# Kernel optimization log

Hardware: AMD Instinct MI355X
Metric: run time of the kernel (lower is better)

## Reference

```python
import jax, jax.numpy as jnp
import numpy as np

NEG_INF = -1e30  # stands in for torch's -inf diagonal mask; exp() underflows to 0 identically


def conv1x1(x, w, b):
    # x: [B,C,H,W], w: [O,C], b: [O]
    return jnp.einsum('oc,bchw->bohw', w, x) + b[None, :, None, None]


def s_module(x, qw, qb, kw, kb, vw, vb, gamma):
    # CCNet criss-cross attention with -inf diagonal masking on the H branch.
    B, C, H, W = x.shape
    q = conv1x1(x, qw, qb)  # [B,C8,H,W]
    k = conv1x1(x, kw, kb)  # [B,C8,H,W]
    v = conv1x1(x, vw, vb)  # [B,C,H,W]
    # energy_H[b,h,w,g] = <q[b,:,h,w], k[b,:,g,w]>  (attend along column)
    e_h = jnp.einsum('bchw,bcgw->bhwg', q, k)
    diag_mask = jnp.where(jnp.eye(H, dtype=bool), NEG_INF, 0.0).astype(x.dtype)
    e_h = e_h + diag_mask[None, :, None, :]  # mask h == g
    # energy_W[b,h,w,v] = <q[b,:,h,w], k[b,:,h,v]>  (attend along row)
    e_w = jnp.einsum('bchw,bchv->bhwv', q, k)
    att = jax.nn.softmax(jnp.concatenate([e_h, e_w], axis=-1), axis=-1)  # [B,H,W,H+W]
    a_h, a_w = att[..., :H], att[..., H:]
    out_h = jnp.einsum('bcgw,bhwg->bchw', v, a_h)
    out_w = jnp.einsum('bchv,bhwv->bchw', v, a_w)
    return gamma * (out_h + out_w) + x


def cam_module(x, fb, gamma):
    # channel attention: energy [B,C,C], max-sub trick, softmax, bmm back
    B, C, H, W = x.shape
    f = fb.reshape(B, C, H * W)
    energy = jnp.einsum('bcn,bdn->bcd', f, f)
    energy_new = jnp.max(energy, axis=-1, keepdims=True) - energy
    att = jax.nn.softmax(energy_new, axis=-1)
    out = jnp.einsum('bcd,bdn->bcn', att, f).reshape(B, C, H, W)
    return x + gamma * out


def _forward(x, fb, w_conv, b_conv, bn_g, bn_b,
             xq_w, xq_b, xk_w, xk_b, xv_w, xv_b, x_gamma,
             fq_w, fq_b, fk_w, fk_b, fv_w, fv_b, f_gamma,
             pam_gamma, pam_gamma2, cam_gamma):
    # MaxPool2d(kernel=2, stride=2)
    fbd = jax.lax.reduce_window(fb, -jnp.inf, jax.lax.max,
                                (1, 1, 2, 2), (1, 1, 2, 2), 'VALID')
    # convblock: 1x1 conv + BatchNorm (training-mode batch stats) + ReLU
    y = conv1x1(fbd, w_conv, b_conv)
    mu = jnp.mean(y, axis=(0, 2, 3), keepdims=True)
    var = jnp.var(y, axis=(0, 2, 3), keepdims=True)
    y = (y - mu) * jax.lax.rsqrt(var + 1e-5)
    y = y * bn_g[None, :, None, None] + bn_b[None, :, None, None]
    y = jax.nn.relu(y)
    # FeedbackSpatialAttention (PAM)
    x_att = pam_gamma * s_module(x, xq_w, xq_b, xk_w, xk_b, xv_w, xv_b, x_gamma)
    fb_att = s_module(y, fq_w, fq_b, fk_w, fk_b, fv_w, fv_b, f_gamma)
    pam_out = x + x_att + pam_gamma2 * fb_att
    # CAM on (x, processed fb)
    cam_out = cam_module(x, y, cam_gamma)
    return pam_out + cam_out


def setup_inputs() -> dict:
    key = jax.random.key(0)
    ks = jax.random.split(key, 24)
    B, C, H, W = 4, 64, 128, 128
    C8 = C // 8
    d = {
        'x': jax.random.normal(ks[0], (B, C, H, W), jnp.float32),
        'fb': jax.random.normal(ks[1], (B, C, 2 * H, 2 * W), jnp.float32),
        'w_conv': jax.random.normal(ks[2], (C, C), jnp.float32) * 0.05,
        'b_conv': jax.random.normal(ks[3], (C,), jnp.float32) * 0.02,
        'bn_g': jax.random.uniform(ks[4], (C,), jnp.float32, 0.5, 1.5),
        'bn_b': jax.random.normal(ks[5], (C,), jnp.float32) * 0.02,
        'xq_w': jax.random.normal(ks[6], (C8, C), jnp.float32) * 0.05,
        'xq_b': jax.random.normal(ks[7], (C8,), jnp.float32) * 0.02,
        'xk_w': jax.random.normal(ks[8], (C8, C), jnp.float32) * 0.05,
        'xk_b': jax.random.normal(ks[9], (C8,), jnp.float32) * 0.02,
        'xv_w': jax.random.normal(ks[10], (C, C), jnp.float32) * 0.05,
        'xv_b': jax.random.normal(ks[11], (C,), jnp.float32) * 0.02,
        'x_gamma': jax.random.normal(ks[12], (1,), jnp.float32) * 0.1,
        'fq_w': jax.random.normal(ks[13], (C8, C), jnp.float32) * 0.05,
        'fq_b': jax.random.normal(ks[14], (C8,), jnp.float32) * 0.02,
        'fk_w': jax.random.normal(ks[15], (C8, C), jnp.float32) * 0.05,
        'fk_b': jax.random.normal(ks[16], (C8,), jnp.float32) * 0.02,
        'fv_w': jax.random.normal(ks[17], (C, C), jnp.float32) * 0.05,
        'fv_b': jax.random.normal(ks[18], (C,), jnp.float32) * 0.02,
        'f_gamma': jax.random.normal(ks[19], (1,), jnp.float32) * 0.1,
        'pam_gamma': jax.random.normal(ks[20], (1,), jnp.float32) * 0.1,
        'pam_gamma2': jax.random.normal(ks[21], (1,), jnp.float32) * 0.1,
        'cam_gamma': jax.random.normal(ks[22], (1,), jnp.float32) * 0.1,
    }
    return d


def reference(x, fb, w_conv, b_conv, bn_g, bn_b,
              xq_w, xq_b, xk_w, xk_b, xv_w, xv_b, x_gamma,
              fq_w, fq_b, fk_w, fk_b, fv_w, fv_b, f_gamma,
              pam_gamma, pam_gamma2, cam_gamma):
    return _forward(x, fb, w_conv, b_conv, bn_g, bn_b,
                    xq_w, xq_b, xk_w, xk_b, xv_w, xv_b, x_gamma,
                    fq_w, fq_b, fk_w, fk_b, fv_w, fv_b, f_gamma,
                    pam_gamma, pam_gamma2, cam_gamma)
```

## Files before the change

### kernel.cpp

```cpp
#include <hip/hip_runtime.h>
#include <hip/hip_bf16.h>

#define NP 16384
#define NB 4

typedef __hip_bfloat16 bf16;
typedef unsigned short u16;
typedef unsigned short us8 __attribute__((ext_vector_type(8)));
typedef short ss8 __attribute__((ext_vector_type(8)));
typedef float f32x4 __attribute__((ext_vector_type(4)));
__device__ __forceinline__ float bf2f(const bf16 v) { return __bfloat162float(v); }
__device__ __forceinline__ bf16 f2bf(float v) { return __float2bfloat16(v); }
__device__ __forceinline__ float bfu(u16 h) {
  return __uint_as_float(((unsigned)h) << 16);
}
__device__ __forceinline__ u16 fbu(float v) {
  bf16 b = f2bf(v);
  return *(u16*)&b;
}


__global__ __launch_bounds__(256) void k_pool_conv(
    const float* __restrict__ fb, const float* __restrict__ wconv,
    const float* __restrict__ bconv, bf16* __restrict__ Y) {
  __shared__ float wS[64 * 65], bS[64], Xs[4096];
  int tid = threadIdx.x;
  int b = blockIdx.x >> 8, tile = blockIdx.x & 255;
  int n0 = tile * 64;
  for (int i = tid; i < 4096; i += 256) wS[(i >> 6) * 65 + (i & 63)] = wconv[i];
  if (tid < 64) bS[tid] = bconv[tid];
  for (int i = tid; i < 4096; i += 256) {
    int c = i >> 6, px = i & 63;
    int n = n0 + px, h = n >> 7, w = n & 127;
    size_t fbase = ((size_t)((b * 64 + c) * 256 + 2 * h)) * 256 + 2 * w;
    float2 v01 = *(const float2*)(fb + fbase);
    float2 v23 = *(const float2*)(fb + fbase + 256);
    Xs[i] = fmaxf(fmaxf(v01.x, v01.y), fmaxf(v23.x, v23.y));
  }
  __syncthreads();
  int ty = tid >> 4, tx = tid & 15;
  float acc[4][4];
#pragma unroll
  for (int i = 0; i < 4; ++i) {
    float bv = bS[ty + 16 * i];
#pragma unroll
    for (int j = 0; j < 4; ++j) acc[i][j] = bv;
  }
  for (int c = 0; c < 64; ++c) {
    float xv[4], wv[4];
#pragma unroll
    for (int j = 0; j < 4; ++j) xv[j] = Xs[c * 64 + tx * 4 + j];
#pragma unroll
    for (int i = 0; i < 4; ++i) wv[i] = wS[(ty + 16 * i) * 65 + c];
#pragma unroll
    for (int i = 0; i < 4; ++i)
#pragma unroll
      for (int j = 0; j < 4; ++j) acc[i][j] = fmaf(wv[i], xv[j], acc[i][j]);
  }
#pragma unroll
  for (int i = 0; i < 4; ++i) {
    int ch = ty + 16 * i;
    bf16* yb = Y + (size_t)(b * 64 + ch) * NP + n0 + tx * 4;
#pragma unroll
    for (int j = 0; j < 4; ++j) yb[j] = f2bf(acc[i][j]);
  }
}

__global__ __launch_bounds__(256) void k_stats_p1(const bf16* __restrict__ Y,
                                                  float* __restrict__ PS) {
  int blk = blockIdx.x, tid = threadIdx.x;
  int o = blk >> 3, slab = blk & 7;
  int b = slab >> 1, half = slab & 1;
  const us8* vp =
      (const us8*)(Y + ((size_t)(b * 64 + o)) * NP + half * 8192);
  float s = 0.f, ss = 0.f;
#pragma unroll
  for (int it = 0; it < 4; ++it) {
    us8 v = vp[tid + 256 * it];
#pragma unroll
    for (int e = 0; e < 8; ++e) {
      float f = bfu(v[e]);
      s += f;
      ss = fmaf(f, f, ss);
    }
  }
  for (int off = 32; off > 0; off >>= 1) {
    s += __shfl_down(s, off, 64);
    ss += __shfl_down(ss, off, 64);
  }
  __shared__ float sh[8];
  int wv = tid >> 6, ln = tid & 63;
  if (ln == 0) { sh[wv] = s; sh[4 + wv] = ss; }
  __syncthreads();
  if (tid == 0) {
    PS[blk] = sh[0] + sh[1] + sh[2] + sh[3];
    PS[512 + blk] = sh[4] + sh[5] + sh[6] + sh[7];
  }
}

__global__ __launch_bounds__(64) void k_stats_p2(
    const float* __restrict__ PS, const float* __restrict__ bng,
    const float* __restrict__ bnb, float* __restrict__ SCALE,
    float* __restrict__ SHIFT, const float* xg, const float* fg,
    const float* pg, const float* pg2, const float* cg,
    float* __restrict__ HDR) {
  int o = threadIdx.x;
  float s = 0.f, ss = 0.f;
#pragma unroll
  for (int k = 0; k < 8; ++k) {
    s += PS[o * 8 + k];
    ss += PS[512 + o * 8 + k];
  }
  const float inv = 1.0f / (NB * NP);
  float mu = s * inv;
  float var = ss * inv - mu * mu;
  float r = rsqrtf(var + 1e-5f);
  float sc = r * bng[o];
  SCALE[o] = sc;
  SHIFT[o] = bnb[o] - mu * sc;
  if (o == 0) {
    float vpg = pg[0];
    HDR[1] = vpg * xg[0];
    HDR[2] = pg2[0] * fg[0];
    HDR[3] = 2.0f + vpg;
    HDR[4] = pg2[0];
    HDR[5] = cg[0];
  }
}

__global__ __launch_bounds__(256) void k_conv80x2(
    const float* __restrict__ xin, const bf16* __restrict__ Yin,
    const float* __restrict__ SCALE, const float* __restrict__ SHIFT,
    const float* __restrict__ qw0, const float* __restrict__ qb0,
    const float* __restrict__ kw0, const float* __restrict__ kb0,
    const float* __restrict__ vw0, const float* __restrict__ vb0,
    const float* __restrict__ qw1, const float* __restrict__ qb1,
    const float* __restrict__ kw1, const float* __restrict__ kb1,
    const float* __restrict__ vw1, const float* __restrict__ vb1,
    bf16* __restrict__ QK, bf16* __restrict__ V) {
  __shared__ float wS[80 * 65], bS[80];
  __shared__ u16 Xs[4096];
  int tid = threadIdx.x;
  int m = blockIdx.x >> 10;
  int rest = blockIdx.x & 1023;
  int b = rest >> 8, tile = rest & 255;
  int n0 = tile * 64;
  const float* qw = m ? qw1 : qw0;
  const float* qb = m ? qb1 : qb0;
  const float* kw = m ? kw1 : kw0;
  const float* kb = m ? kb1 : kb0;
  const float* vw = m ? vw1 : vw0;
  const float* vb = m ? vb1 : vb0;
  for (int i = tid; i < 512; i += 256) {
    wS[(i >> 6) * 65 + (i & 63)] = qw[i];
    wS[(8 + (i >> 6)) * 65 + (i & 63)] = kw[i];
  }
  for (int i = tid; i < 4096; i += 256)
    wS[(16 + (i >> 6)) * 65 + (i & 63)] = vw[i];
  if (tid < 8) { bS[tid] = qb[tid]; bS[8 + tid] = kb[tid]; }
  if (tid < 64) bS[16 + tid] = vb[tid];
  for (int i = tid; i < 4096; i += 256) {
    int c = i >> 6, px = i & 63;
    size_t idx = (size_t)(b * 64 + c) * NP + n0 + px;
    float v;
    if (m) {
      v = bf2f(Yin[idx]);
      v = fmaf(v, SCALE[c], SHIFT[c]);
      v = fmaxf(v, 0.f);
    } else {
      v = xin[idx];
    }
    Xs[i] = fbu(v);
  }
  __syncthreads();
  int ty = tid >> 4, tx = tid & 15;
  float acc[5][4];
#pragma unroll
  for (int i = 0; i < 5; ++i) {
    float bv = bS[ty + 16 * i];
#pragma unroll
    for (int j = 0; j < 4; ++j) acc[i][j] = bv;
  }
  for (int c = 0; c < 64; ++c) {
    float xv[4], wv[5];
#pragma unroll
    for (int j = 0; j < 4; ++j) xv[j] = bfu(Xs[c * 64 + tx * 4 + j]);
#pragma unroll
    for (int i = 0; i < 5; ++i) wv[i] = wS[(ty + 16 * i) * 65 + c];
#pragma unroll
    for (int i = 0; i < 5; ++i)
#pragma unroll
      for (int j = 0; j < 4; ++j) acc[i][j] = fmaf(wv[i], xv[j], acc[i][j]);
  }
#pragma unroll
  for (int i = 0; i < 5; ++i) {
    int ch = ty + 16 * i;
    bf16* dst;
    size_t base;
    if (ch < 8) {
      dst = QK; base = (size_t)(((m * 2 + 0) * 4 + b) * 8 + ch) * NP;
    } else if (ch < 16) {
      dst = QK; base = (size_t)(((m * 2 + 1) * 4 + b) * 8 + (ch - 8)) * NP;
    } else {
      dst = V; base = (size_t)((m * 4 + b) * 64 + (ch - 16)) * NP;
    }
#pragma unroll
    for (int j = 0; j < 4; ++j) dst[base + n0 + tx * 4 + j] = f2bf(acc[i][j]);
  }
}

__global__ __launch_bounds__(256) void k_transpose2(
    const u16* __restrict__ inA, u16* __restrict__ outA,
    const u16* __restrict__ inB, u16* __restrict__ outB, int nA) {
  int tileId = blockIdx.x & 15;
  int plane = blockIdx.x >> 4;
  const u16* ip;
  u16* op;
  if (plane < nA) {
    ip = inA + (size_t)plane * NP;
    op = outA + (size_t)plane * NP;
  } else {
    ip = inB + (size_t)(plane - nA) * NP;
    op = outB + (size_t)(plane - nA) * NP;
  }
  int th = tileId >> 2, tw = tileId & 3;
  __shared__ u16 t[32][33];
  int lx = threadIdx.x & 31, ly = threadIdx.x >> 5;
  for (int i = 0; i < 32; i += 8)
    t[ly + i][lx] = ip[(size_t)(th * 32 + ly + i) * 128 + tw * 32 + lx];
  __syncthreads();
  for (int i = 0; i < 32; i += 8)
    op[(size_t)(tw * 32 + ly + i) * 128 + th * 32 + lx] = t[lx][ly + i];
}

__global__ __launch_bounds__(256, 4) void k_av(
    const bf16* __restrict__ QK, const bf16* __restrict__ QKT,
    const bf16* __restrict__ V, const bf16* __restrict__ VT,
    float* __restrict__ MWp, float* __restrict__ LWp,
    float* __restrict__ MHp, float* __restrict__ LHp,
    float* __restrict__ OW, bf16* __restrict__ OHT) {
  int blk = blockIdx.x;
  int m = blk & 1, mode = (blk >> 1) & 1;
  int bid = blk >> 2;
  int b = bid >> 7, h = bid & 127;
  const bf16* qkbase = mode ? QKT : QK;
  const bf16* Qp = qkbase + (size_t)(((m * 2 + 0) * 4 + b) * 8) * NP;
  const bf16* Kp = qkbase + (size_t)(((m * 2 + 1) * 4 + b) * 8) * NP;
  const bf16* Vp = (mode ? VT : V) + (size_t)((m * 4 + b) * 64) * NP;
  __shared__ __align__(16) u16 qT[128 * 8];
  __shared__ __align__(16) u16 kT[128 * 8];
  __shared__ __align__(16) u16 Vs[64 * 136];
  int tid = threadIdx.x;
  {
    int c = (tid >> 4) & 7, vj = tid & 15;
    const bf16* src = (tid < 128) ? Qp : Kp;
    u16* dst = (tid < 128) ? qT : kT;
    const us8* sp = (const us8*)(src + (size_t)c * NP + (size_t)h * 128);
    us8 sv = sp[vj];
#pragma unroll
    for (int e = 0; e < 8; ++e) {
      int j = vj * 8 + e;
      int p = ((j & 7) << 4) | (j >> 3);
      dst[p * 8 + c] = sv[e];
    }
  }
  for (int i2 = tid; i2 < 1024; i2 += 256) {
    int c = i2 >> 4, vj = i2 & 15;
    const us8* vp = (const us8*)(Vp + (size_t)c * NP + (size_t)h * 128);
    us8 vv = vp[vj];
    *(us8*)&Vs[c * 136 + vj * 8] = vv;
  }
  __syncthreads();
  int lane = tid & 63, wv = tid >> 6;
  int il = lane & 15, gq = lane >> 4;
  size_t sb = (size_t)(m * 4 + b) * NP;
  float* owBase = OW + (size_t)((m * 4 + b) * 64) * NP + (size_t)h * 128;
  bf16* ohBase = OHT + (size_t)((m * 4 + b) * 64) * NP + (size_t)h * 128;
#pragma unroll
  for (int sub = 0; sub < 2; ++sub) {
    int ib = wv * 32 + sub * 16;
    int i = ib + il;
    int pi = ((i & 7) << 4) | (i >> 3);
    us8 qv = *(const us8*)&qT[pi * 8];
    float qr[8];
#pragma unroll
    for (int c = 0; c < 8; ++c) qr[c] = bfu(qv[c]);
    float scr[4][8];
    float mrow = -3.0e38f;
#pragma unroll
    for (int ks = 0; ks < 4; ++ks) {
#pragma unroll
      for (int e = 0; e < 8; ++e) {
        int j = ks * 32 + gq * 8 + e;
        int pj = ((j & 7) << 4) | (j >> 3);
        us8 kv = *(const us8*)&kT[pj * 8];
        float s = 0.f;
#pragma unroll
        for (int c = 0; c < 8; ++c) s = fmaf(qr[c], bfu(kv[c]), s);
        if (mode && j == i) s = -1.0e30f;
        scr[ks][e] = s;
        mrow = fmaxf(mrow, s);
      }
    }
    mrow = fmaxf(mrow, __shfl_xor(mrow, 16, 64));
    mrow = fmaxf(mrow, __shfl_xor(mrow, 32, 64));
    float l = 0.f;
    ss8 afr[4];
#pragma unroll
    for (int ks = 0; ks < 4; ++ks) {
      ss8 af;
#pragma unroll
      for (int e = 0; e < 8; ++e) {
        float ev = __expf(scr[ks][e] - mrow);
        l += ev;
        af[e] = (short)fbu(ev);
      }
      afr[ks] = af;
    }
    l += __shfl_xor(l, 16, 64);
    l += __shfl_xor(l, 32, 64);
    if (gq == 0) {
      if (mode == 0) {
        MWp[sb + (size_t)h * 128 + i] = mrow;
        LWp[sb + (size_t)h * 128 + i] = l;
      } else {
        MHp[sb + (size_t)i * 128 + h] = mrow;
        LHp[sb + (size_t)i * 128 + h] = l;
      }
    }
#pragma unroll
    for (int ct = 0; ct < 4; ++ct) {
      f32x4 acc = {0.f, 0.f, 0.f, 0.f};
#pragma unroll
      for (int ks = 0; ks < 4; ++ks) {
        ss8 bv = *(const ss8*)&Vs[(ct * 16 + il) * 136 + ks * 32 + gq * 8];
        acc = __builtin_amdgcn_mfma_f32_16x16x32_bf16(afr[ks], bv, acc, 0, 0, 0);
      }
      int cch = ct * 16 + il;
      int i0 = ib + gq * 4;
      if (mode == 0) {
#pragma unroll
        for (int r = 0; r < 4; ++r)
          owBase[(size_t)cch * NP + (size_t)(i0 + r)] = acc[r];
      } else {
#pragma unroll
        for (int r = 0; r < 4; ++r)
          ohBase[(size_t)cch * NP + (size_t)(i0 + r)] = f2bf(acc[r]);
      }
    }
  }
}

__global__ __launch_bounds__(256) void k_merge2(
    const bf16* __restrict__ OHT, const float* __restrict__ OW,
    const float* __restrict__ MWp, const float* __restrict__ LWp,
    const float* __restrict__ MHp, const float* __restrict__ LHp,
    const float* __restrict__ HDR, float* __restrict__ ACC) {
  int tileId = blockIdx.x & 15;
  int plane = blockIdx.x >> 4;
  int b = plane >> 6;
  int th = tileId >> 2, tw = tileId & 3;
  __shared__ float t0[32][33], t1[32][33];
  int lx = threadIdx.x & 31, ly = threadIdx.x >> 5;
  const bf16* ip0 = OHT + (size_t)plane * NP;
  const bf16* ip1 = OHT + (size_t)(256 + plane) * NP;
  for (int i = 0; i < 32; i += 8) {
    size_t idx = (size_t)(th * 32 + ly + i) * 128 + tw * 32 + lx;
    t0[ly + i][lx] = bf2f(ip0[idx]);
    t1[ly + i][lx] = bf2f(ip1[idx]);
  }
  __syncthreads();
  float sc0 = HDR[1], sc1 = HDR[2];
  float* op = ACC + (size_t)plane * NP;
  const float* ow0 = OW + (size_t)plane * NP;
  const float* ow1 = OW + (size_t)(256 + plane) * NP;
  size_t s0 = (size_t)b * NP, s1 = (size_t)(4 + b) * NP;
  for (int i = 0; i < 32; i += 8) {
    int hh = tw * 32 + ly + i, ww = th * 32 + lx;
    size_t idx = (size_t)hh * 128 + ww;
    float mw0 = MWp[s0 + idx], mh0 = MHp[s0 + idx];
    float M0 = fmaxf(mw0, mh0);
    float ea0 = __expf(mw0 - M0), eb0 = __expf(mh0 - M0);
    float inv0 = 1.0f / (LWp[s0 + idx] * ea0 + LHp[s0 + idx] * eb0);
    float v0 = (ea0 * ow0[idx] + eb0 * t0[lx][ly + i]) * inv0;
    float mw1 = MWp[s1 + idx], mh1 = MHp[s1 + idx];
    float M1 = fmaxf(mw1, mh1);
    float ea1 = __expf(mw1 - M1), eb1 = __expf(mh1 - M1);
    float inv1 = 1.0f / (LWp[s1 + idx] * ea1 + LHp[s1 + idx] * eb1);
    float v1 = (ea1 * ow1[idx] + eb1 * t1[lx][ly + i]) * inv1;
    op[idx] = sc0 * v0 + sc1 * v1;
  }
}

__global__ __launch_bounds__(256) void k_gram(const bf16* __restrict__ Y,
                                              const float* __restrict__ SCALE,
                                              const float* __restrict__ SHIFT,
                                              float* __restrict__ GP) {
  int b = blockIdx.x >> 7, ch = (blockIdx.x >> 2) & 31, t = blockIdx.x & 3;
  int tid = threadIdx.x;
  __shared__ float fs[64 * 129];
  int cg = tid >> 4, dg = tid & 15;
  float acc[4][4];
#pragma unroll
  for (int i = 0; i < 4; ++i)
#pragma unroll
    for (int jx = 0; jx < 4; ++jx) acc[i][jx] = 0.f;
  const bf16* yb = Y + (size_t)b * 64 * NP + ch * 512;
  for (int idx = tid; idx < 8192; idx += 256) {
    int c = idx >> 7, j = idx & 127;
    float v = fmaf(bf2f(yb[(size_t)c * NP + t * 128 + j]), SCALE[c], SHIFT[c]);
    fs[c * 129 + j] = fmaxf(v, 0.f);
  }
  __syncthreads();
  for (int j = 0; j < 128; ++j) {
    float a[4], d[4];
#pragma unroll
    for (int i = 0; i < 4; ++i) a[i] = fs[(cg * 4 + i) * 129 + j];
#pragma unroll
    for (int i = 0; i < 4; ++i) d[i] = fs[(dg * 4 + i) * 129 + j];
#pragma unroll
    for (int i = 0; i < 4; ++i)
#pragma unroll
      for (int jx = 0; jx < 4; ++jx) acc[i][jx] = fmaf(a[i], d[jx], acc[i][jx]);
  }
  float* gp = GP + ((size_t)(b * 128) + ch * 4 + t) * 4096;
#pragma unroll
  for (int i = 0; i < 4; ++i)
#pragma unroll
    for (int jx = 0; jx < 4; ++jx)
      gp[(cg * 4 + i) * 64 + dg * 4 + jx] = acc[i][jx];
}

__global__ __launch_bounds__(256) void k_gram_reduce(const float* __restrict__ GP,
                                                     float* __restrict__ CATT) {
  int b = blockIdx.x >> 4, rg = blockIdx.x & 15;
  int tid = threadIdx.x;
  __shared__ float Es[256];
  int e = rg * 256 + tid;
  float s = 0.f;
  for (int k = 0; k < 128; ++k) s += GP[((size_t)b * 128 + k) * 4096 + e];
  Es[tid] = s;
  __syncthreads();
  int wv = tid >> 6, ln = tid & 63;
  float v = Es[wv * 64 + ln];
  float mn = v;
  for (int off = 32; off; off >>= 1) mn = fminf(mn, __shfl_xor(mn, off, 64));
  float ev = __expf(mn - v);
  float ssum = ev;
  for (int off = 32; off; off >>= 1) ssum += __shfl_xor(ssum, off, 64);
  CATT[((size_t)b * 64 + rg * 4 + wv) * 64 + ln] = ev / ssum;
}

__global__ __launch_bounds__(256) void k_final(
    const float* __restrict__ x, const bf16* __restrict__ Y,
    const float* __restrict__ SCALE, const float* __restrict__ SHIFT,
    const float* __restrict__ CATT, const float* __restrict__ HDR,
    float* __restrict__ OUT) {
  __shared__ float attS[64 * 65], Ys[64 * 65];
  int tid = threadIdx.x;
  int b = blockIdx.x >> 8, tile = blockIdx.x & 255;
  int n0 = tile * 64;
  for (int i = tid; i < 4096; i += 256)
    attS[(i >> 6) * 65 + (i & 63)] = CATT[(size_t)b * 4096 + i];
  for (int i = tid; i < 4096; i += 256) {
    int d = i >> 6, px = i & 63;
    float v = fmaf(bf2f(Y[(size_t)(b * 64 + d) * NP + n0 + px]), SCALE[d], SHIFT[d]);
    Ys[d * 65 + px] = fmaxf(v, 0.f);
  }
  __syncthreads();
  int cg = tid >> 4, pgx = tid & 15;
  int c0 = cg * 4, p0 = pgx * 4;
  float acc[4][4];
#pragma unroll
  for (int i = 0; i < 4; ++i)
#pragma unroll
    for (int j = 0; j < 4; ++j) acc[i][j] = 0.f;
  for (int d = 0; d < 64; ++d) {
    float a[4], yv[4];
#pragma unroll
    for (int i = 0; i < 4; ++i) a[i] = attS[(c0 + i) * 65 + d];
#pragma unroll
    for (int j = 0; j < 4; ++j) yv[j] = Ys[d * 65 + p0 + j];
#pragma unroll
    for (int i = 0; i < 4; ++i)
#pragma unroll
      for (int j = 0; j < 4; ++j) acc[i][j] = fmaf(a[i], yv[j], acc[i][j]);
  }
  float c2pg = HDR[3], fpg2 = HDR[4], fcg = HDR[5];
#pragma unroll
  for (int i = 0; i < 4; ++i) {
    size_t base = (size_t)(b * 64 + c0 + i) * NP + n0 + p0;
#pragma unroll
    for (int j = 0; j < 4; ++j) {
      float yv = Ys[(c0 + i) * 65 + p0 + j];
      OUT[base + j] =
          c2pg * x[base + j] + fpg2 * yv + OUT[base + j] + fcg * acc[i][j];
    }
  }
}

extern "C" void kernel_launch(void* const* d_in, const int* in_sizes, int n_in,
                              void* d_out, int out_size, void* d_ws, size_t ws_size,
                              hipStream_t stream) {
  const float* x = (const float*)d_in[0];
  const float* fbp = (const float*)d_in[1];

  char* base = (char*)d_ws;
  float* HDR = (float*)base;
  float* SCALE = HDR + 16;
  float* SHIFT = SCALE + 64;
  char* p = base + 4096;
  bf16* Y = (bf16*)p;    p += 8388608;
  bf16* QK = (bf16*)p;   p += 4194304;
  bf16* QKT = (bf16*)p;  p += 4194304;
  bf16* V = (bf16*)p;    p += 16777216;
  bf16* VT = (bf16*)p;   p += 16777216;
  float* MWp = (float*)p; p += 524288;
  float* LWp = (float*)p; p += 524288;
  float* MHp = (float*)p; p += 524288;
  float* LHp = (float*)p; p += 524288;
  bf16* OHT = (bf16*)p;  p += 16777216;
  float* OW = (float*)p; p += 33554432;
  float* GP = (float*)p; p += 8388608;
  float* CATT = (float*)p; p += 1048576;
  float* ACC = (float*)d_out;
  float* PS = (float*)QK;

  k_pool_conv<<<1024, 256, 0, stream>>>(fbp, (const float*)d_in[2],
                                        (const float*)d_in[3], Y);
  k_stats_p1<<<512, 256, 0, stream>>>(Y, PS);
  k_stats_p2<<<1, 64, 0, stream>>>(PS, (const float*)d_in[4],
                                   (const float*)d_in[5], SCALE, SHIFT,
                                   (const float*)d_in[12], (const float*)d_in[19],
                                   (const float*)d_in[20], (const float*)d_in[21],
                                   (const float*)d_in[22], HDR);

  k_conv80x2<<<2048, 256, 0, stream>>>(
      x, Y, SCALE, SHIFT,
      (const float*)d_in[6], (const float*)d_in[7], (const float*)d_in[8],
      (const float*)d_in[9], (const float*)d_in[10], (const float*)d_in[11],
      (const float*)d_in[13], (const float*)d_in[14], (const float*)d_in[15],
      (const float*)d_in[16], (const float*)d_in[17], (const float*)d_in[18],
      QK, V);
  k_transpose2<<<10240, 256, 0, stream>>>((const u16*)QK, (u16*)QKT,
                                          (const u16*)V, (u16*)VT, 128);
  k_av<<<2048, 256, 0, stream>>>(QK, QKT, V, VT, MWp, LWp, MHp, LHp, OW, OHT);
  k_merge2<<<4096, 256, 0, stream>>>(OHT, OW, MWp, LWp, MHp, LHp, HDR, ACC);

  k_gram<<<512, 256, 0, stream>>>(Y, SCALE, SHIFT, GP);
  k_gram_reduce<<<64, 256, 0, stream>>>(GP, CATT);
  k_final<<<1024, 256, 0, stream>>>(x, Y, SCALE, SHIFT, CATT, HDR,
                                    (float*)d_out);
}
```

Before: 301.3 us.

## Rewrite fused QKV 1x1 conv with bf16 MFMA and hi/lo split weights

Replaces the scalar-FMA 80-output 1x1 conv kernel with one using MFMA 16x16x32 bf16 instructions. Weights are split into hi and lo bf16 parts to keep near-fp32 weight precision. Activations are staged in XOR-swizzled LDS with vectorized global loads, and each block covers 128 pixels so the grid is halved. Stores are vectorized 4-wide. The aim is to cut the VALU-bound conv cost, in exchange for extra LDS and swizzle complexity.

```diff
diff --git a/kernel.cpp b/kernel.cpp
--- a/kernel.cpp
+++ b/kernel.cpp
@@ -7,6 +7,7 @@
 typedef __hip_bfloat16 bf16;
 typedef unsigned short u16;
 typedef unsigned short us8 __attribute__((ext_vector_type(8)));
+typedef unsigned short us4 __attribute__((ext_vector_type(4)));
 typedef short ss8 __attribute__((ext_vector_type(8)));
 typedef float f32x4 __attribute__((ext_vector_type(4)));
 __device__ __forceinline__ float bf2f(const bf16 v) { return __bfloat162float(v); }
@@ -128,7 +129,7 @@
   }
 }
 
-__global__ __launch_bounds__(256) void k_conv80x2(
+__global__ __launch_bounds__(256, 4) void k_conv_mfma(
     const float* __restrict__ xin, const bf16* __restrict__ Yin,
     const float* __restrict__ SCALE, const float* __restrict__ SHIFT,
     const float* __restrict__ qw0, const float* __restrict__ qb0,
@@ -138,74 +139,102 @@
     const float* __restrict__ kw1, const float* __restrict__ kb1,
     const float* __restrict__ vw1, const float* __restrict__ vb1,
     bf16* __restrict__ QK, bf16* __restrict__ V) {
-  __shared__ float wS[80 * 65], bS[80];
-  __shared__ u16 Xs[4096];
+  __shared__ __align__(16) u16 Xs[128 * 64];
+  __shared__ __align__(16) u16 wHi[80 * 64], wLo[80 * 64];
+  __shared__ float bS[80];
   int tid = threadIdx.x;
-  int m = blockIdx.x >> 10;
-  int rest = blockIdx.x & 1023;
-  int b = rest >> 8, tile = rest & 255;
-  int n0 = tile * 64;
+  int m = blockIdx.x >> 9;
+  int b = (blockIdx.x >> 7) & 3;
+  int tile = blockIdx.x & 127;
+  int n0 = tile * 128;
   const float* qw = m ? qw1 : qw0;
   const float* qb = m ? qb1 : qb0;
   const float* kw = m ? kw1 : kw0;
   const float* kb = m ? kb1 : kb0;
   const float* vw = m ? vw1 : vw0;
   const float* vb = m ? vb1 : vb0;
-  for (int i = tid; i < 512; i += 256) {
-    wS[(i >> 6) * 65 + (i & 63)] = qw[i];
-    wS[(8 + (i >> 6)) * 65 + (i & 63)] = kw[i];
-  }
-  for (int i = tid; i < 4096; i += 256)
-    wS[(16 + (i >> 6)) * 65 + (i & 63)] = vw[i];
-  if (tid < 8) { bS[tid] = qb[tid]; bS[8 + tid] = kb[tid]; }
-  if (tid < 64) bS[16 + tid] = vb[tid];
-  for (int i = tid; i < 4096; i += 256) {
-    int c = i >> 6, px = i & 63;
-    size_t idx = (size_t)(b * 64 + c) * NP + n0 + px;
-    float v;
-    if (m) {
-      v = bf2f(Yin[idx]);
-      v = fmaf(v, SCALE[c], SHIFT[c]);
-      v = fmaxf(v, 0.f);
-    } else {
-      v = xin[idx];
-    }
-    Xs[i] = fbu(v);
-  }
-  __syncthreads();
-  int ty = tid >> 4, tx = tid & 15;
-  float acc[5][4];
-#pragma unroll
-  for (int i = 0; i < 5; ++i) {
-    float bv = bS[ty + 16 * i];
-#pragma unroll
-    for (int j = 0; j < 4; ++j) acc[i][j] = bv;
-  }
-  for (int c = 0; c < 64; ++c) {
-    float xv[4], wv[5];
-#pragma unroll
-    for (int j = 0; j < 4; ++j) xv[j] = bfu(Xs[c * 64 + tx * 4 + j]);
-#pragma unroll
-    for (int i = 0; i < 5; ++i) wv[i] = wS[(ty + 16 * i) * 65 + c];
-#pragma unroll
-    for (int i = 0; i < 5; ++i)
-#pragma unroll
-      for (int j = 0; j < 4; ++j) acc[i][j] = fmaf(wv[i], xv[j], acc[i][j]);
-  }
-#pragma unroll
-  for (int i = 0; i < 5; ++i) {
-    int ch = ty + 16 * i;
+  for (int i = tid; i < 5120; i += 256) {
+    int oc = i >> 6, c = i & 63;
+    float w;
+    if (oc < 8) w = qw[oc * 64 + c];
+    else if (oc < 16) w = kw[(oc - 8) * 64 + c];
+    else w = vw[(oc - 16) * 64 + c];
+    u16 hb = fbu(w);
+    u16 lb = fbu(w - bfu(hb));
+    int idx = (oc * 64 + c) ^ ((oc & 7) << 3);
+    wHi[idx] = hb;
+    wLo[idx] = lb;
+  }
+  if (tid < 80)
+    bS[tid] = (tid < 8) ? qb[tid] : (tid < 16) ? kb[tid - 8] : vb[tid - 16];
+  if (m) {
+    for (int i2 = tid; i2 < 1024; i2 += 256) {
+      int c = i2 >> 4, vj = i2 & 15;
+      us8 v = *(const us8*)(Yin + (size_t)(b * 64 + c) * NP + n0 + vj * 8);
+      float sc = SCALE[c], sh = SHIFT[c];
+#pragma unroll
+      for (int e = 0; e < 8; ++e) {
+        int px = vj * 8 + e;
+        float f = fmaxf(fmaf(bfu(v[e]), sc, sh), 0.f);
+        Xs[(px * 64 + c) ^ ((((px & 7) ^ ((px >> 3) & 7))) << 3)] = fbu(f);
+      }
+    }
+  } else {
+    for (int i2 = tid; i2 < 2048; i2 += 256) {
+      int c = i2 >> 5, vj = i2 & 31;
+      float4 v = *(const float4*)(xin + (size_t)(b * 64 + c) * NP + n0 + vj * 4);
+      float vv[4] = {v.x, v.y, v.z, v.w};
+#pragma unroll
+      for (int r = 0; r < 4; ++r) {
+        int px = vj * 4 + r;
+        Xs[(px * 64 + c) ^ ((((px & 7) ^ ((px >> 3) & 7))) << 3)] = fbu(vv[r]);
+      }
+    }
+  }
+  __syncthreads();
+  int lane = tid & 63, wv = tid >> 6;
+  int il = lane & 15, gq = lane >> 4;
+  int pxb = wv * 32;
+  ss8 afr[2][2];
+#pragma unroll
+  for (int sub = 0; sub < 2; ++sub)
+#pragma unroll
+    for (int ks = 0; ks < 2; ++ks) {
+      int px = pxb + sub * 16 + il;
+      int idx =
+          (px * 64 + ks * 32 + gq * 8) ^ ((((px & 7) ^ ((px >> 3) & 7))) << 3);
+      afr[sub][ks] = *(const ss8*)&Xs[idx];
+    }
+#pragma unroll
+  for (int oct = 0; oct < 5; ++oct) {
+    int oc = oct * 16 + il;
+    ss8 wh[2], wl[2];
+#pragma unroll
+    for (int ks = 0; ks < 2; ++ks) {
+      int idx = (oc * 64 + ks * 32 + gq * 8) ^ ((oc & 7) << 3);
+      wh[ks] = *(const ss8*)&wHi[idx];
+      wl[ks] = *(const ss8*)&wLo[idx];
+    }
+    float bv = bS[oc];
     bf16* dst;
-    size_t base;
-    if (ch < 8) {
-      dst = QK; base = (size_t)(((m * 2 + 0) * 4 + b) * 8 + ch) * NP;
-    } else if (ch < 16) {
-      dst = QK; base = (size_t)(((m * 2 + 1) * 4 + b) * 8 + (ch - 8)) * NP;
-    } else {
-      dst = V; base = (size_t)((m * 4 + b) * 64 + (ch - 16)) * NP;
-    }
-#pragma unroll
-    for (int j = 0; j < 4; ++j) dst[base + n0 + tx * 4 + j] = f2bf(acc[i][j]);
+    size_t basep;
+    if (oc < 8) { dst = QK; basep = (size_t)(((m * 2 + 0) * 4 + b) * 8 + oc) * NP; }
+    else if (oc < 16) { dst = QK; basep = (size_t)(((m * 2 + 1) * 4 + b) * 8 + (oc - 8)) * NP; }
+    else { dst = V; basep = (size_t)((m * 4 + b) * 64 + (oc - 16)) * NP; }
+#pragma unroll
+    for (int sub = 0; sub < 2; ++sub) {
+      f32x4 acc = {bv, bv, bv, bv};
+#pragma unroll
+      for (int ks = 0; ks < 2; ++ks) {
+        acc = __builtin_amdgcn_mfma_f32_16x16x32_bf16(afr[sub][ks], wh[ks], acc, 0, 0, 0);
+        acc = __builtin_amdgcn_mfma_f32_16x16x32_bf16(afr[sub][ks], wl[ks], acc, 0, 0, 0);
+      }
+      int px0 = pxb + sub * 16 + gq * 4;
+      us4 ov;
+#pragma unroll
+      for (int r = 0; r < 4; ++r) ov[r] = fbu(acc[r]);
+      *(us4*)(dst + basep + n0 + px0) = ov;
+    }
   }
 }
 
@@ -535,7 +564,7 @@
                                    (const float*)d_in[20], (const float*)d_in[21],
                                    (const float*)d_in[22], HDR);
 
-  k_conv80x2<<<2048, 256, 0, stream>>>(
+  k_conv_mfma<<<1024, 256, 0, stream>>>(
       x, Y, SCALE, SHIFT,
       (const float*)d_in[6], (const float*)d_in[7], (const float*)d_in[8],
       (const float*)d_in[9], (const float*)d_in[10], (const float*)d_in[11],
```

New measurement: 282.8 us. 1.07x faster.
